# Kernel optimization log

Measured on AMD Instinct MI355X. Metric: run time of the kernel, lower is better.

## Reference

```python
import jax, jax.numpy as jnp
import numpy as np

N, E = 50000, 600000
IN, H, C = 128, 128, 10


def _glorot(key, shape):
    lim = float(np.sqrt(6.0 / (shape[0] + shape[1])))
    return jax.random.uniform(key, shape, jnp.float32, -lim, lim)


def setup_inputs() -> dict:
    key = jax.random.key(0)
    ks = jax.random.split(key, 16)
    inp = {
        "x": jax.random.normal(ks[0], (N, IN), jnp.float32),
        "edge_index": jax.random.randint(ks[1], (2, E), 0, N, jnp.int64)
        if jax.config.jax_enable_x64 else jax.random.randint(ks[1], (2, E), 0, N, jnp.int32),
        "W1": _glorot(ks[2], (IN, H)), "b1": jnp.zeros((H,), jnp.float32),
        "W2": _glorot(ks[3], (H, H)),  "b2": jnp.zeros((H,), jnp.float32),
        "W3": _glorot(ks[4], (H, H)),  "b3": jnp.zeros((H,), jnp.float32),
        "W4": _glorot(ks[5], (H, H)),  "b4": jnp.zeros((H,), jnp.float32),
        "Wm1": _glorot(ks[6], (H, H)), "bm1": jnp.zeros((H,), jnp.float32),
        "Wm2": _glorot(ks[7], (H, C)), "bm2": jnp.zeros((C,), jnp.float32),
    }
    return inp


def gcn_layer(x, W, b, src, dst):
    # PyG GCNConv: linear transform, add self-loops, symmetric normalization,
    # scatter-add aggregation to destination nodes, then bias.
    n = x.shape[0]
    xw = x @ W  # [N, H]
    # in-degree (computed on dst), +1 for self-loop
    deg = jax.ops.segment_sum(jnp.ones(src.shape[0], xw.dtype), dst, num_segments=n) + 1.0
    dinv = jax.lax.rsqrt(deg)  # deg >= 1, safe
    norm = dinv[src] * dinv[dst]  # [E]
    agg = jax.ops.segment_sum(xw[src] * norm[:, None], dst, num_segments=n)
    agg = agg + xw * (dinv * dinv)[:, None]  # self-loop messages
    return agg + b


def reference(x, edge_index, W1, b1, W2, b2, W3, b3, W4, b4, Wm1, bm1, Wm2, bm2):
    src, dst = edge_index[0], edge_index[1]
    h = jax.nn.elu(gcn_layer(x, W1, b1, src, dst))
    h = jax.nn.elu(gcn_layer(h, W2, b2, src, dst))
    h = jax.nn.elu(gcn_layer(h, W3, b3, src, dst))
    h = jax.nn.elu(gcn_layer(h, W4, b4, src, dst))
    # Faithful to the source bug: S is reassigned from the fixed `s = h` each
    # iteration, so only the last MLP layer's output survives.
    s = h
    for Wm, bm in ((Wm1, bm1), (Wm2, bm2)):
        S = jax.nn.elu(s @ Wm + bm)
    return (h, S)
```

## Files before the change

kernel.cpp:

```cpp
#include <hip/hip_runtime.h>
#include <hip/hip_bf16.h>
#include <math.h>

typedef __hip_bfloat16 bf16;
typedef __attribute__((ext_vector_type(8))) short short8;
typedef __attribute__((ext_vector_type(4))) float f32x4;

__device__ __forceinline__ float elu_f(float x){ return x > 0.f ? x : expm1f(x); }
__device__ __forceinline__ float b2f(unsigned short u){ return __uint_as_float(((unsigned)u) << 16); }
__device__ __forceinline__ unsigned short f2b(float f){ bf16 h = __float2bfloat16(f); return *reinterpret_cast<unsigned short*>(&h); }

__global__ __launch_bounds__(256) void detect_part_kernel(const unsigned* __restrict__ ei_u, int twoE_words,
                                                          const unsigned* __restrict__ x_u, int min_xwords,
                                                          int* __restrict__ raw){
    __shared__ int sd[256];
    __shared__ int sc[256];
    int tid = threadIdx.x;
    int gid = blockIdx.x*256 + tid;
    long long pairs = twoE_words/2;

    int orv = 0;
    if (gid < 16384 && pairs > 0){
        long long idx = ((long long)gid * pairs) / 16384;
        long long w = 2*idx + 1;
        if (w < twoE_words) orv = (int)ei_u[w];
    }
    int cnt = 0;
    int s = gid - 16384;
    if (s >= 0 && s < 4096){
        long long idx = ((long long)s * min_xwords) / 4096;
        if (idx < min_xwords){
            unsigned e = (x_u[idx] >> 7) & 0xFFu;
            cnt = (e >= 96u && e <= 160u) ? 1 : 0;
        }
    }
    sd[tid] = orv; sc[tid] = cnt;
    __syncthreads();
    #pragma unroll
    for (int off = 128; off > 0; off >>= 1){
        if (tid < off){ sd[tid] |= sd[tid+off]; sc[tid] += sc[tid+off]; }
        __syncthreads();
    }
    if (tid == 0){
        if (sd[0]) atomicOr(&raw[0], sd[0]);
        if (sc[0]) atomicAdd(&raw[1], sc[0]);
    }
}

__global__ void finalize_kernel(const int* __restrict__ raw, int* __restrict__ flags){
    flags[0] = (raw[0] == 0) ? 1 : 0;
    flags[1] = (raw[1]*2 > 4096) ? 1 : 0;
}

__device__ __forceinline__ int load_src(const int* ei, int e, int E, int is64){
    return is64 ? ei[2*e] : ei[e];
}
__device__ __forceinline__ int load_dst(const int* ei, int e, int E, int is64){
    return is64 ? ei[2*(E + e)] : ei[E + e];
}
__device__ __forceinline__ float loadf(const void* base, size_t idx, int isbf){
    return isbf ? __bfloat162float(((const bf16*)base)[idx]) : ((const float*)base)[idx];
}

__global__ void count_kernel(const int* __restrict__ ei, const int* __restrict__ flags,
                             int* __restrict__ counts, int E, int N){
    int e = blockIdx.x*256 + threadIdx.x;
    if (e < E){
        int d = load_dst(ei, e, E, flags[0]);
        if ((unsigned)d < (unsigned)N) atomicAdd(&counts[d], 1);
    }
}

__global__ void partial_kernel(const int* __restrict__ counts, int* __restrict__ partial, int N){
    __shared__ int sd[256];
    int tid = threadIdx.x;
    int i = blockIdx.x*256 + tid;
    sd[tid] = (i < N) ? counts[i] : 0;
    __syncthreads();
    #pragma unroll
    for (int off = 128; off > 0; off >>= 1){
        if (tid < off) sd[tid] += sd[tid+off];
        __syncthreads();
    }
    if (tid == 0) partial[blockIdx.x] = sd[0];
}

__global__ void scanp_kernel(const int* __restrict__ partial, int* __restrict__ blockoff, int nb){
    __shared__ int sd[256];
    int tid = threadIdx.x;
    int v = (tid < nb) ? partial[tid] : 0;
    sd[tid] = v;
    __syncthreads();
    #pragma unroll
    for (int off = 1; off < 256; off <<= 1){
        int t = (tid >= off) ? sd[tid-off] : 0;
        __syncthreads();
        sd[tid] += t;
        __syncthreads();
    }
    if (tid < nb) blockoff[tid] = sd[tid] - v;
}

__global__ void offsets_kernel(const int* __restrict__ counts, const int* __restrict__ blockoff,
                               int* __restrict__ offsets, int* __restrict__ cursor,
                               float* __restrict__ dinv, int N){
    __shared__ int sd[256];
    int tid = threadIdx.x;
    int i = blockIdx.x*256 + tid;
    int v = (i < N) ? counts[i] : 0;
    sd[tid] = v;
    __syncthreads();
    #pragma unroll
    for (int off = 1; off < 256; off <<= 1){
        int t = (tid >= off) ? sd[tid-off] : 0;
        __syncthreads();
        sd[tid] += t;
        __syncthreads();
    }
    if (i < N){
        int o = blockoff[blockIdx.x] + sd[tid] - v;
        offsets[i] = o;
        cursor[i]  = o;
        double d = (double)(v + 1);
        if (d < 1.0) d = 1.0;
        dinv[i] = (float)(1.0 / sqrt(d));
    }
}

__global__ void scatter_kernel(const int* __restrict__ ei, const int* __restrict__ flags,
                               int* __restrict__ cursor, int* __restrict__ csr, int E, int N){
    int e = blockIdx.x*256 + threadIdx.x;
    if (e < E){
        int is64 = flags[0];
        int d = load_dst(ei, e, E, is64);
        int s = load_src(ei, e, E, is64);
        if ((unsigned)d < (unsigned)N){
            int pos = atomicAdd(&cursor[d], 1);
            if ((unsigned)pos < (unsigned)E) csr[pos] = s;
        }
    }
}

__global__ __launch_bounds__(256) void wprep_kernel(const void* __restrict__ W0, const void* __restrict__ W1,
                                                    const void* __restrict__ W2, const void* __restrict__ W3,
                                                    const int* __restrict__ flags,
                                                    unsigned short* __restrict__ WThi, unsigned short* __restrict__ WTlo){
    const void* Wl = blockIdx.x == 0 ? W0 : blockIdx.x == 1 ? W1 : blockIdx.x == 2 ? W2 : W3;
    int isbf = flags[1];
    unsigned short* dh = WThi + (size_t)blockIdx.x*16384;
    unsigned short* dl = WTlo + (size_t)blockIdx.x*16384;
    for (int i = threadIdx.x; i < 16384; i += 256){
        int k = i >> 7, c = i & 127;
        unsigned short hi, lo;
        if (isbf){
            hi = ((const unsigned short*)Wl)[i]; lo = 0;
        } else {
            float w = ((const float*)Wl)[i];
            hi = f2b(w);
            lo = f2b(w - b2f(hi));
        }
        dh[c*128 + k] = hi;
        dl[c*128 + k] = lo;
    }
}

__global__ __launch_bounds__(256) void gemm_kernel(const void* __restrict__ X,
                                                   const unsigned short* __restrict__ WThi,
                                                   const unsigned short* __restrict__ WTlo,
                                                   const int* __restrict__ flags,
                                                   void* __restrict__ Y, int N){
    __shared__ __align__(16) unsigned short xhi[64*136];
    __shared__ __align__(16) unsigned short xlo[64*136];
    __shared__ __align__(16) unsigned short bh[128*40];
    __shared__ __align__(16) unsigned short bl[128*40];
    int tid = threadIdx.x;
    int r0 = blockIdx.x*64;
    int isbf = flags[1];

    if (isbf){
        for (int i = tid; i < 64*16; i += 256){
            int r = i >> 4, sg = i & 15;
            float4 v = make_float4(0.f,0.f,0.f,0.f);
            if (r0 + r < N) v = ((const float4*)X)[(size_t)(r0+r)*16 + sg];
            *(float4*)&xhi[r*136 + sg*8] = v;
        }
    } else {
        for (int i = tid; i < 64*32; i += 256){
            int r = i >> 5, f4 = i & 31;
            float4 v = make_float4(0.f,0.f,0.f,0.f);
            if (r0 + r < N) v = ((const float4*)X)[(size_t)(r0+r)*32 + f4];
            ushort4 hv, lv;
            hv.x = f2b(v.x); lv.x = f2b(v.x - b2f(hv.x));
            hv.y = f2b(v.y); lv.y = f2b(v.y - b2f(hv.y));
            hv.z = f2b(v.z); lv.z = f2b(v.z - b2f(hv.z));
            hv.w = f2b(v.w); lv.w = f2b(v.w - b2f(hv.w));
            *(ushort4*)&xhi[r*136 + f4*4] = hv;
            *(ushort4*)&xlo[r*136 + f4*4] = lv;
        }
    }

    int wv = tid >> 6, lane = tid & 63;
    int lq = lane & 15, lh = lane >> 4;

    f32x4 acc[8];
    #pragma unroll
    for (int i = 0; i < 8; i++){
        #pragma unroll
        for (int e = 0; e < 4; e++) acc[i][e] = 0.f;
    }

    for (int k0 = 0; k0 < 4; k0++){
        __syncthreads();
        for (int i = tid; i < 512; i += 256){
            int rr = i >> 2, sg = i & 3;
            *(float4*)&bh[rr*40 + sg*8] = *(const float4*)&WThi[rr*128 + k0*32 + sg*8];
        }
        if (!isbf){
            for (int i = tid; i < 512; i += 256){
                int rr = i >> 2, sg = i & 3;
                *(float4*)&bl[rr*40 + sg*8] = *(const float4*)&WTlo[rr*128 + k0*32 + sg*8];
            }
        }
        __syncthreads();

        short8 ah = *reinterpret_cast<const short8*>(&xhi[(wv*16 + lq)*136 + k0*32 + lh*8]);
        if (isbf){
            #pragma unroll
            for (int nt = 0; nt < 8; nt++){
                short8 bhf = *reinterpret_cast<const short8*>(&bh[(nt*16 + lq)*40 + lh*8]);
                acc[nt] = __builtin_amdgcn_mfma_f32_16x16x32_bf16(ah, bhf, acc[nt], 0, 0, 0);
            }
        } else {
            short8 al = *reinterpret_cast<const short8*>(&xlo[(wv*16 + lq)*136 + k0*32 + lh*8]);
            #pragma unroll
            for (int nt = 0; nt < 8; nt++){
                short8 bhf = *reinterpret_cast<const short8*>(&bh[(nt*16 + lq)*40 + lh*8]);
                short8 blf = *reinterpret_cast<const short8*>(&bl[(nt*16 + lq)*40 + lh*8]);
                acc[nt] = __builtin_amdgcn_mfma_f32_16x16x32_bf16(ah, bhf, acc[nt], 0, 0, 0);
                acc[nt] = __builtin_amdgcn_mfma_f32_16x16x32_bf16(al, bhf, acc[nt], 0, 0, 0);
                acc[nt] = __builtin_amdgcn_mfma_f32_16x16x32_bf16(ah, blf, acc[nt], 0, 0, 0);
            }
        }
    }

    if (isbf){
        bf16* Yb = (bf16*)Y;
        #pragma unroll
        for (int nt = 0; nt < 8; nt++){
            #pragma unroll
            for (int i = 0; i < 4; i++){
                int row = r0 + wv*16 + lh*4 + i;
                if (row < N) Yb[(size_t)row*128 + nt*16 + lq] = __float2bfloat16(acc[nt][i]);
            }
        }
    } else {
        float* Yf = (float*)Y;
        #pragma unroll
        for (int nt = 0; nt < 8; nt++){
            #pragma unroll
            for (int i = 0; i < 4; i++){
                int row = r0 + wv*16 + lh*4 + i;
                if (row < N) Yf[(size_t)row*128 + nt*16 + lq] = acc[nt][i];
            }
        }
    }
}

__global__ __launch_bounds__(256) void agg_kernel(const void* __restrict__ XW, const float* __restrict__ dinv,
                                                  const int* __restrict__ offsets, const int* __restrict__ counts,
                                                  const int* __restrict__ csr, const void* __restrict__ bias,
                                                  void* __restrict__ Hout, const int* __restrict__ flags, int N){
    int wave = threadIdx.x >> 6;
    int lane = threadIdx.x & 63;
    int n = blockIdx.x*4 + wave;
    if (n >= N) return;
    int isbf = flags[1];

    float dn = dinv[n];
    float sw = dn*dn;

    if (isbf){
        int h = lane >> 5, q = lane & 31;
        const ushort4* X4 = (const ushort4*)XW;
        float a0, a1, a2, a3;
        if (h == 0){
            ushort4 v = X4[(size_t)n*32 + q];
            a0 = b2f(v.x)*sw; a1 = b2f(v.y)*sw; a2 = b2f(v.z)*sw; a3 = b2f(v.w)*sw;
        } else { a0 = a1 = a2 = a3 = 0.f; }

        int j0 = offsets[n], cnt = counts[n];
        for (int base = 0; base < cnt; base += 64){
            int m = cnt - base; if (m > 64) m = 64;
            int s_l = 0; float w_l = 0.f;
            if (lane < m){
                int s = csr[j0 + base + lane];
                if ((unsigned)s < (unsigned)N){ s_l = s; w_l = dinv[s]*dn; }
            }
            int j = 0;
            for (; j + 8 <= m; j += 8){
                int   s0 = __shfl(s_l, j + h),     s1 = __shfl(s_l, j + 2 + h);
                int   s2 = __shfl(s_l, j + 4 + h), s3 = __shfl(s_l, j + 6 + h);
                float w0 = __shfl(w_l, j + h),     w1 = __shfl(w_l, j + 2 + h);
                float w2 = __shfl(w_l, j + 4 + h), w3 = __shfl(w_l, j + 6 + h);
                ushort4 u0 = X4[(size_t)s0*32 + q];
                ushort4 u1 = X4[(size_t)s1*32 + q];
                ushort4 u2 = X4[(size_t)s2*32 + q];
                ushort4 u3 = X4[(size_t)s3*32 + q];
                a0 += b2f(u0.x)*w0; a1 += b2f(u0.y)*w0; a2 += b2f(u0.z)*w0; a3 += b2f(u0.w)*w0;
                a0 += b2f(u1.x)*w1; a1 += b2f(u1.y)*w1; a2 += b2f(u1.z)*w1; a3 += b2f(u1.w)*w1;
                a0 += b2f(u2.x)*w2; a1 += b2f(u2.y)*w2; a2 += b2f(u2.z)*w2; a3 += b2f(u2.w)*w2;
                a0 += b2f(u3.x)*w3; a1 += b2f(u3.y)*w3; a2 += b2f(u3.z)*w3; a3 += b2f(u3.w)*w3;
            }
            for (; j < m; j += 2){
                int   s = __shfl(s_l, j + h);
                float w = __shfl(w_l, j + h);
                ushort4 u = X4[(size_t)s*32 + q];
                a0 += b2f(u.x)*w; a1 += b2f(u.y)*w; a2 += b2f(u.z)*w; a3 += b2f(u.w)*w;
            }
        }
        a0 += __shfl_xor(a0, 32);
        a1 += __shfl_xor(a1, 32);
        a2 += __shfl_xor(a2, 32);
        a3 += __shfl_xor(a3, 32);
        if (h == 0){
            a0 = elu_f(a0 + loadf(bias, 4*q + 0, 1));
            a1 = elu_f(a1 + loadf(bias, 4*q + 1, 1));
            a2 = elu_f(a2 + loadf(bias, 4*q + 2, 1));
            a3 = elu_f(a3 + loadf(bias, 4*q + 3, 1));
            ushort4 o;
            o.x = f2b(a0); o.y = f2b(a1); o.z = f2b(a2); o.w = f2b(a3);
            ((ushort4*)Hout)[(size_t)n*32 + q] = o;
        }
    } else {
        float accx, accy;
        float2 v = ((const float2*)XW)[(size_t)n*64 + lane];
        accx = v.x*sw; accy = v.y*sw;

        int j0 = offsets[n], cnt = counts[n];
        for (int base = 0; base < cnt; base += 64){
            int m = cnt - base; if (m > 64) m = 64;
            int s_l = 0; float w_l = 0.f;
            if (lane < m){
                int s = csr[j0 + base + lane];
                if ((unsigned)s < (unsigned)N){ s_l = s; w_l = dinv[s]*dn; }
            }
            int j = 0;
            const float2* XF = (const float2*)XW;
            for (; j + 4 <= m; j += 4){
                int   s0 = __shfl(s_l, j),   s1 = __shfl(s_l, j+1), s2 = __shfl(s_l, j+2), s3 = __shfl(s_l, j+3);
                float w0 = __shfl(w_l, j),   w1 = __shfl(w_l, j+1), w2 = __shfl(w_l, j+2), w3 = __shfl(w_l, j+3);
                float2 u0 = XF[(size_t)s0*64 + lane];
                float2 u1 = XF[(size_t)s1*64 + lane];
                float2 u2 = XF[(size_t)s2*64 + lane];
                float2 u3 = XF[(size_t)s3*64 + lane];
                accx += u0.x*w0; accy += u0.y*w0;
                accx += u1.x*w1; accy += u1.y*w1;
                accx += u2.x*w2; accy += u2.y*w2;
                accx += u3.x*w3; accy += u3.y*w3;
            }
            for (; j < m; ++j){
                int   s = __shfl(s_l, j);
                float w = __shfl(w_l, j);
                float2 u = XF[(size_t)s*64 + lane];
                accx += u.x*w; accy += u.y*w;
            }
        }

        accx = elu_f(accx + loadf(bias, lane*2,     0));
        accy = elu_f(accy + loadf(bias, lane*2 + 1, 0));
        *(float2*)((float*)Hout + (size_t)n*128 + lane*2) = make_float2(accx, accy);
    }
}

__global__ __launch_bounds__(256) void mlp_kernel(void* __restrict__ dout, const void* __restrict__ Wm,
                                                  const void* __restrict__ bm, const int* __restrict__ flags, int N){
    __shared__ float ws_[1280];
    __shared__ __align__(16) float hs[16][136];
    int tid = threadIdx.x;
    int isbf = flags[1];
    for (int i = tid; i < 1280; i += 256) ws_[i] = loadf(Wm, i, isbf);

    int r = tid >> 4, c = tid & 15;
    int row = blockIdx.x*16 + r;
    if (isbf){
        if (row < N){
            float4 v = ((const float4*)dout)[(size_t)row*16 + c];
            const unsigned short* u = (const unsigned short*)&v;
            #pragma unroll
            for (int j = 0; j < 8; j++) hs[r][c*8 + j] = b2f(u[j]);
        }
    } else {
        if (row < N){
            float4 v0 = ((const float4*)dout)[(size_t)row*32 + c*2];
            float4 v1 = ((const float4*)dout)[(size_t)row*32 + c*2 + 1];
            *(float4*)&hs[r][c*8]     = v0;
            *(float4*)&hs[r][c*8 + 4] = v1;
        }
    }
    __syncthreads();
    if (row < N && c < 10){
        float acc = 0.f;
        #pragma unroll 8
        for (int k = 0; k < 128; k++) acc += hs[r][k]*ws_[k*10 + c];
        acc += loadf(bm, c, isbf);
        float res = elu_f(acc);
        if (isbf){
            ((bf16*)dout)[(size_t)N*128 + (size_t)row*10 + c] = __float2bfloat16(res);
        } else {
            ((float*)dout)[(size_t)N*128 + (size_t)row*10 + c] = res;
        }
    }
}

static inline char* alignup(char* p, size_t a){ return (char*)(((uintptr_t)p + a - 1) & ~(a - 1)); }

extern "C" void kernel_launch(void* const* d_in, const int* in_sizes, int n_in,
                              void* d_out, int out_size, void* d_ws, size_t ws_size,
                              hipStream_t stream){
    const void* x  = d_in[0];
    const int*  ei = (const int*)d_in[1];
    const void* W[4] = {d_in[2], d_in[4], d_in[6], d_in[8]};
    const void* B[4] = {d_in[3], d_in[5], d_in[7], d_in[9]};
    const void* Wm2 = d_in[12];
    const void* bm2 = d_in[13];

    int N = in_sizes[0] / 128;
    int E = in_sizes[1] / 2;

    char* p = (char*)d_ws;
    int*   flags    = (int*)p;
    int*   raw      = flags + 2;                   p = alignup(p + 4*sizeof(int), 256);
    float* dinv     = (float*)p;                   p = alignup(p + (size_t)N*4, 256);
    int*   counts   = (int*)p;                     p = alignup(p + (size_t)N*4, 256);
    int*   offsets  = (int*)p;                     p = alignup(p + (size_t)N*4, 256);
    int*   cursor   = (int*)p;                     p = alignup(p + (size_t)N*4, 256);
    int*   partial  = (int*)p;                     p = alignup(p + 256*4, 256);
    int*   blockoff = (int*)p;                     p = alignup(p + 256*4, 256);
    int*   csr      = (int*)p;                     p = alignup(p + (size_t)E*4, 256);
    void*  xw       = (void*)p;                    p = alignup(p + (size_t)N*128*4, 256);
    unsigned short* WThi = (unsigned short*)p;     p = alignup(p + (size_t)4*16384*2, 256);
    unsigned short* WTlo = (unsigned short*)p;     p = alignup(p + (size_t)4*16384*2, 256);

    int nb = (N + 255)/256;

    hipMemsetAsync(flags, 0, 4*sizeof(int), stream);
    hipMemsetAsync(counts, 0, (size_t)N*sizeof(int), stream);
    detect_part_kernel<<<128, 256, 0, stream>>>((const unsigned*)ei, 2*E, (const unsigned*)x, N*128/2, raw);
    finalize_kernel   <<<1, 1, 0, stream>>>(raw, flags);
    wprep_kernel  <<<4, 256, 0, stream>>>(W[0], W[1], W[2], W[3], flags, WThi, WTlo);
    count_kernel  <<<(E + 255)/256, 256, 0, stream>>>(ei, flags, counts, E, N);
    partial_kernel<<<nb, 256, 0, stream>>>(counts, partial, N);
    scanp_kernel  <<<1, 256, 0, stream>>>(partial, blockoff, nb);
    offsets_kernel<<<nb, 256, 0, stream>>>(counts, blockoff, offsets, cursor, dinv, N);
    scatter_kernel<<<(E + 255)/256, 256, 0, stream>>>(ei, flags, cursor, csr, E, N);

    for (int l = 0; l < 4; ++l){
        const void* Xin = (l == 0) ? x : (const void*)d_out;
        gemm_kernel<<<(N + 63)/64, 256, 0, stream>>>(Xin, WThi + (size_t)l*16384, WTlo + (size_t)l*16384, flags, xw, N);
        agg_kernel <<<(N + 3)/4, 256, 0, stream>>>(xw, dinv, offsets, counts, csr, B[l], d_out, flags, N);
    }
    mlp_kernel<<<((N*16) + 255)/256, 256, 0, stream>>>(d_out, Wm2, bm2, flags, N);
}
```

Measured before the change: 503.0 us.

## Store intermediate XW in fp16 and unify aggregation path; parallelize weight prep

The GEMM now always writes its per-layer output XW as fp16 instead of fp32 (or bf16). The aggregation kernel gathers half2 pairs per lane, which halves the bytes of the random neighbor gathers in the default fp32 path. The weight-transpose prep is also split across 256 blocks instead of 4. The cost is reduced precision of the intermediate, with fp16 range and rounding risk against an fp32 reference.

Result: faster. 409.2 us (-18.6%).

```diff
diff --git a/kernel.cpp b/kernel.cpp
--- a/kernel.cpp
+++ b/kernel.cpp
@@ -1,5 +1,6 @@
 #include <hip/hip_runtime.h>
 #include <hip/hip_bf16.h>
+#include <hip/hip_fp16.h>
 #include <math.h>
 
 typedef __hip_bfloat16 bf16;
@@ -9,6 +10,10 @@
 __device__ __forceinline__ float elu_f(float x){ return x > 0.f ? x : expm1f(x); }
 __device__ __forceinline__ float b2f(unsigned short u){ return __uint_as_float(((unsigned)u) << 16); }
 __device__ __forceinline__ unsigned short f2b(float f){ bf16 h = __float2bfloat16(f); return *reinterpret_cast<unsigned short*>(&h); }
+__device__ __forceinline__ float2 h2f2(unsigned u){
+    __half2 h = *reinterpret_cast<__half2*>(&u);
+    return make_float2(__low2float(h), __high2float(h));
+}
 
 __global__ __launch_bounds__(256) void detect_part_kernel(const unsigned* __restrict__ ei_u, int twoE_words,
                                                           const unsigned* __restrict__ x_u, int min_xwords,
@@ -145,30 +150,28 @@
                                                     const void* __restrict__ W2, const void* __restrict__ W3,
                                                     const int* __restrict__ flags,
                                                     unsigned short* __restrict__ WThi, unsigned short* __restrict__ WTlo){
-    const void* Wl = blockIdx.x == 0 ? W0 : blockIdx.x == 1 ? W1 : blockIdx.x == 2 ? W2 : W3;
+    int l = blockIdx.x >> 6;
+    const void* Wl = l == 0 ? W0 : l == 1 ? W1 : l == 2 ? W2 : W3;
     int isbf = flags[1];
-    unsigned short* dh = WThi + (size_t)blockIdx.x*16384;
-    unsigned short* dl = WTlo + (size_t)blockIdx.x*16384;
-    for (int i = threadIdx.x; i < 16384; i += 256){
-        int k = i >> 7, c = i & 127;
-        unsigned short hi, lo;
-        if (isbf){
-            hi = ((const unsigned short*)Wl)[i]; lo = 0;
-        } else {
-            float w = ((const float*)Wl)[i];
-            hi = f2b(w);
-            lo = f2b(w - b2f(hi));
-        }
-        dh[c*128 + k] = hi;
-        dl[c*128 + k] = lo;
-    }
+    int o = (blockIdx.x & 63)*256 + threadIdx.x;
+    int c = o >> 7, k = o & 127;
+    unsigned short hi, lo;
+    if (isbf){
+        hi = ((const unsigned short*)Wl)[k*128 + c]; lo = 0;
+    } else {
+        float w = ((const float*)Wl)[k*128 + c];
+        hi = f2b(w);
+        lo = f2b(w - b2f(hi));
+    }
+    WThi[(size_t)l*16384 + o] = hi;
+    WTlo[(size_t)l*16384 + o] = lo;
 }
 
 __global__ __launch_bounds__(256) void gemm_kernel(const void* __restrict__ X,
                                                    const unsigned short* __restrict__ WThi,
                                                    const unsigned short* __restrict__ WTlo,
                                                    const int* __restrict__ flags,
-                                                   void* __restrict__ Y, int N){
+                                                   __half* __restrict__ Y, int N){
     __shared__ __align__(16) unsigned short xhi[64*136];
     __shared__ __align__(16) unsigned short xlo[64*136];
     __shared__ __align__(16) unsigned short bh[128*40];
@@ -243,30 +246,17 @@
         }
     }
 
-    if (isbf){
-        bf16* Yb = (bf16*)Y;
+    #pragma unroll
+    for (int nt = 0; nt < 8; nt++){
         #pragma unroll
-        for (int nt = 0; nt < 8; nt++){
-            #pragma unroll
-            for (int i = 0; i < 4; i++){
-                int row = r0 + wv*16 + lh*4 + i;
-                if (row < N) Yb[(size_t)row*128 + nt*16 + lq] = __float2bfloat16(acc[nt][i]);
-            }
-        }
-    } else {
-        float* Yf = (float*)Y;
-        #pragma unroll
-        for (int nt = 0; nt < 8; nt++){
-            #pragma unroll
-            for (int i = 0; i < 4; i++){
-                int row = r0 + wv*16 + lh*4 + i;
-                if (row < N) Yf[(size_t)row*128 + nt*16 + lq] = acc[nt][i];
-            }
-        }
-    }
-}
-
-__global__ __launch_bounds__(256) void agg_kernel(const void* __restrict__ XW, const float* __restrict__ dinv,
+        for (int i = 0; i < 4; i++){
+            int row = r0 + wv*16 + lh*4 + i;
+            if (row < N) Y[(size_t)row*128 + nt*16 + lq] = __float2half(acc[nt][i]);
+        }
+    }
+}
+
+__global__ __launch_bounds__(256) void agg_kernel(const unsigned* __restrict__ XWh, const float* __restrict__ dinv,
                                                   const int* __restrict__ offsets, const int* __restrict__ counts,
                                                   const int* __restrict__ csr, const void* __restrict__ bias,
                                                   void* __restrict__ Hout, const int* __restrict__ flags, int N){
@@ -279,95 +269,46 @@
     float dn = dinv[n];
     float sw = dn*dn;
 
+    float2 sf = h2f2(XWh[(size_t)n*64 + lane]);
+    float accx = sf.x*sw, accy = sf.y*sw;
+
+    int j0 = offsets[n], cnt = counts[n];
+    for (int base = 0; base < cnt; base += 64){
+        int m = cnt - base; if (m > 64) m = 64;
+        int s_l = 0; float w_l = 0.f;
+        if (lane < m){
+            int s = csr[j0 + base + lane];
+            if ((unsigned)s < (unsigned)N){ s_l = s; w_l = dinv[s]*dn; }
+        }
+        int j = 0;
+        for (; j + 4 <= m; j += 4){
+            int   s0 = __shfl(s_l, j),   s1 = __shfl(s_l, j+1), s2 = __shfl(s_l, j+2), s3 = __shfl(s_l, j+3);
+            float w0 = __shfl(w_l, j),   w1 = __shfl(w_l, j+1), w2 = __shfl(w_l, j+2), w3 = __shfl(w_l, j+3);
+            unsigned u0 = XWh[(size_t)s0*64 + lane];
+            unsigned u1 = XWh[(size_t)s1*64 + lane];
+            unsigned u2 = XWh[(size_t)s2*64 + lane];
+            unsigned u3 = XWh[(size_t)s3*64 + lane];
+            float2 f0 = h2f2(u0), f1 = h2f2(u1), f2 = h2f2(u2), f3 = h2f2(u3);
+            accx += f0.x*w0; accy += f0.y*w0;
+            accx += f1.x*w1; accy += f1.y*w1;
+            accx += f2.x*w2; accy += f2.y*w2;
+            accx += f3.x*w3; accy += f3.y*w3;
+        }
+        for (; j < m; ++j){
+            int   s = __shfl(s_l, j);
+            float w = __shfl(w_l, j);
+            float2 f = h2f2(XWh[(size_t)s*64 + lane]);
+            accx += f.x*w; accy += f.y*w;
+        }
+    }
+
+    accx = elu_f(accx + loadf(bias, 2*lane,     isbf));
+    accy = elu_f(accy + loadf(bias, 2*lane + 1, isbf));
     if (isbf){
-        int h = lane >> 5, q = lane & 31;
-        const ushort4* X4 = (const ushort4*)XW;
-        float a0, a1, a2, a3;
-        if (h == 0){
-            ushort4 v = X4[(size_t)n*32 + q];
-            a0 = b2f(v.x)*sw; a1 = b2f(v.y)*sw; a2 = b2f(v.z)*sw; a3 = b2f(v.w)*sw;
-        } else { a0 = a1 = a2 = a3 = 0.f; }
-
-        int j0 = offsets[n], cnt = counts[n];
-        for (int base = 0; base < cnt; base += 64){
-            int m = cnt - base; if (m > 64) m = 64;
-            int s_l = 0; float w_l = 0.f;
-            if (lane < m){
-                int s = csr[j0 + base + lane];
-                if ((unsigned)s < (unsigned)N){ s_l = s; w_l = dinv[s]*dn; }
-            }
-            int j = 0;
-            for (; j + 8 <= m; j += 8){
-                int   s0 = __shfl(s_l, j + h),     s1 = __shfl(s_l, j + 2 + h);
-                int   s2 = __shfl(s_l, j + 4 + h), s3 = __shfl(s_l, j + 6 + h);
-                float w0 = __shfl(w_l, j + h),     w1 = __shfl(w_l, j + 2 + h);
-                float w2 = __shfl(w_l, j + 4 + h), w3 = __shfl(w_l, j + 6 + h);
-                ushort4 u0 = X4[(size_t)s0*32 + q];
-                ushort4 u1 = X4[(size_t)s1*32 + q];
-                ushort4 u2 = X4[(size_t)s2*32 + q];
-                ushort4 u3 = X4[(size_t)s3*32 + q];
-                a0 += b2f(u0.x)*w0; a1 += b2f(u0.y)*w0; a2 += b2f(u0.z)*w0; a3 += b2f(u0.w)*w0;
-                a0 += b2f(u1.x)*w1; a1 += b2f(u1.y)*w1; a2 += b2f(u1.z)*w1; a3 += b2f(u1.w)*w1;
-                a0 += b2f(u2.x)*w2; a1 += b2f(u2.y)*w2; a2 += b2f(u2.z)*w2; a3 += b2f(u2.w)*w2;
-                a0 += b2f(u3.x)*w3; a1 += b2f(u3.y)*w3; a2 += b2f(u3.z)*w3; a3 += b2f(u3.w)*w3;
-            }
-            for (; j < m; j += 2){
-                int   s = __shfl(s_l, j + h);
-                float w = __shfl(w_l, j + h);
-                ushort4 u = X4[(size_t)s*32 + q];
-                a0 += b2f(u.x)*w; a1 += b2f(u.y)*w; a2 += b2f(u.z)*w; a3 += b2f(u.w)*w;
-            }
-        }
-        a0 += __shfl_xor(a0, 32);
-        a1 += __shfl_xor(a1, 32);
-        a2 += __shfl_xor(a2, 32);
-        a3 += __shfl_xor(a3, 32);
-        if (h == 0){
-            a0 = elu_f(a0 + loadf(bias, 4*q + 0, 1));
-            a1 = elu_f(a1 + loadf(bias, 4*q + 1, 1));
-            a2 = elu_f(a2 + loadf(bias, 4*q + 2, 1));
-            a3 = elu_f(a3 + loadf(bias, 4*q + 3, 1));
-            ushort4 o;
-            o.x = f2b(a0); o.y = f2b(a1); o.z = f2b(a2); o.w = f2b(a3);
-            ((ushort4*)Hout)[(size_t)n*32 + q] = o;
-        }
+        ushort2 o;
+        o.x = f2b(accx); o.y = f2b(accy);
+        *(ushort2*)((bf16*)Hout + (size_t)n*128 + lane*2) = o;
     } else {
-        float accx, accy;
-        float2 v = ((const float2*)XW)[(size_t)n*64 + lane];
-        accx = v.x*sw; accy = v.y*sw;
-
-        int j0 = offsets[n], cnt = counts[n];
-        for (int base = 0; base < cnt; base += 64){
-            int m = cnt - base; if (m > 64) m = 64;
-            int s_l = 0; float w_l = 0.f;
-            if (lane < m){
-                int s = csr[j0 + base + lane];
-                if ((unsigned)s < (unsigned)N){ s_l = s; w_l = dinv[s]*dn; }
-            }
-            int j = 0;
-            const float2* XF = (const float2*)XW;
-            for (; j + 4 <= m; j += 4){
-                int   s0 = __shfl(s_l, j),   s1 = __shfl(s_l, j+1), s2 = __shfl(s_l, j+2), s3 = __shfl(s_l, j+3);
-                float w0 = __shfl(w_l, j),   w1 = __shfl(w_l, j+1), w2 = __shfl(w_l, j+2), w3 = __shfl(w_l, j+3);
-                float2 u0 = XF[(size_t)s0*64 + lane];
-                float2 u1 = XF[(size_t)s1*64 + lane];
-                float2 u2 = XF[(size_t)s2*64 + lane];
-                float2 u3 = XF[(size_t)s3*64 + lane];
-                accx += u0.x*w0; accy += u0.y*w0;
-                accx += u1.x*w1; accy += u1.y*w1;
-                accx += u2.x*w2; accy += u2.y*w2;
-                accx += u3.x*w3; accy += u3.y*w3;
-            }
-            for (; j < m; ++j){
-                int   s = __shfl(s_l, j);
-                float w = __shfl(w_l, j);
-                float2 u = XF[(size_t)s*64 + lane];
-                accx += u.x*w; accy += u.y*w;
-            }
-        }
-
-        accx = elu_f(accx + loadf(bias, lane*2,     0));
-        accy = elu_f(accy + loadf(bias, lane*2 + 1, 0));
         *(float2*)((float*)Hout + (size_t)n*128 + lane*2) = make_float2(accx, accy);
     }
 }
@@ -437,7 +378,7 @@
     int*   partial  = (int*)p;                     p = alignup(p + 256*4, 256);
     int*   blockoff = (int*)p;                     p = alignup(p + 256*4, 256);
     int*   csr      = (int*)p;                     p = alignup(p + (size_t)E*4, 256);
-    void*  xw       = (void*)p;                    p = alignup(p + (size_t)N*128*4, 256);
+    __half* xw      = (__half*)p;                  p = alignup(p + (size_t)N*128*4, 256);
     unsigned short* WThi = (unsigned short*)p;     p = alignup(p + (size_t)4*16384*2, 256);
     unsigned short* WTlo = (unsigned short*)p;     p = alignup(p + (size_t)4*16384*2, 256);
 
@@ -447,7 +388,7 @@
     hipMemsetAsync(counts, 0, (size_t)N*sizeof(int), stream);
     detect_part_kernel<<<128, 256, 0, stream>>>((const unsigned*)ei, 2*E, (const unsigned*)x, N*128/2, raw);
     finalize_kernel   <<<1, 1, 0, stream>>>(raw, flags);
-    wprep_kernel  <<<4, 256, 0, stream>>>(W[0], W[1], W[2], W[3], flags, WThi, WTlo);
+    wprep_kernel  <<<256, 256, 0, stream>>>(W[0], W[1], W[2], W[3], flags, WThi, WTlo);
     count_kernel  <<<(E + 255)/256, 256, 0, stream>>>(ei, flags, counts, E, N);
     partial_kernel<<<nb, 256, 0, stream>>>(counts, partial, N);
     scanp_kernel  <<<1, 256, 0, stream>>>(partial, blockoff, nb);
@@ -457,7 +398,7 @@
     for (int l = 0; l < 4; ++l){
         const void* Xin = (l == 0) ? x : (const void*)d_out;
         gemm_kernel<<<(N + 63)/64, 256, 0, stream>>>(Xin, WThi + (size_t)l*16384, WTlo + (size_t)l*16384, flags, xw, N);
-        agg_kernel <<<(N + 3)/4, 256, 0, stream>>>(xw, dinv, offsets, counts, csr, B[l], d_out, flags, N);
+        agg_kernel <<<(N + 3)/4, 256, 0, stream>>>((const unsigned*)xw, dinv, offsets, counts, csr, B[l], d_out, flags, N);
     }
     mlp_kernel<<<((N*16) + 255)/256, 256, 0, stream>>>(d_out, Wm2, bm2, flags, N);
 }
```
